# Performance work log

Hardware: AMD Instinct MI355X
Metric: run time of the kernel (lower is better)

Reference implementation:

```python
import jax, jax.numpy as jnp
import numpy as np

B = 8                                   # point clouds per batch
NS = [65536, 16384, 4096, 1024, 256]    # points per scale (stride-4 downsampling)
CS = [32, 64, 128, 256, 512]            # encoder channels per scale
K = 3
BN_EPS = 1e-5


def setup_inputs() -> dict:
    key = jax.random.key(0)
    ks = iter(jax.random.split(key, 64))
    inp = {}
    for i, (n, c) in enumerate(zip(NS, CS)):
        inp[f"p{i}"] = jax.random.uniform(next(ks), (n, 3), jnp.float32)
        inp[f"f{i}"] = jax.random.normal(next(ks), (n, c), jnp.float32)
        inp[f"b{i}"] = jnp.repeat(jnp.arange(B, dtype=jnp.int32), n // B)
    # FP stage mlps: a:(4->3) [768,256,256], b:(3->2) [384,128,128],
    #               c:(2->1) [192,64,64],   d:(1->0) [96,32,32]
    cfg = {"a": (CS[3] + CS[4], CS[3]), "b": (CS[2] + CS[3], CS[2]),
           "c": (CS[1] + CS[2], CS[1]), "d": (CS[0] + CS[1], CS[0])}
    for s, (cin, ch) in cfg.items():
        for j, ci in ((1, cin), (2, ch)):
            inp[f"w{s}{j}"] = jax.random.normal(next(ks), (ci, ch), jnp.float32) / float(np.sqrt(ci))
            inp[f"bias{s}{j}"] = jnp.zeros((ch,), jnp.float32)
            inp[f"g{s}{j}"] = jnp.ones((ch,), jnp.float32)
            inp[f"bt{s}{j}"] = jnp.zeros((ch,), jnp.float32)
    return inp


def _knn_interpolate(x2, p2, p1):
    """torch_geometric.nn.knn_interpolate with k=3; equal-sized sorted batches."""
    n1, n2, c = p1.shape[0] // B, p2.shape[0] // B, x2.shape[1]
    p1b, p2b = p1.reshape(B, n1, 3), p2.reshape(B, n2, 3)
    x2b = x2.reshape(B, n2, c)
    # squared dists via |a|^2 + |b|^2 - 2ab (avoids [B,n1,n2,3] temporary)
    d2 = (jnp.sum(p1b * p1b, -1)[:, :, None] + jnp.sum(p2b * p2b, -1)[:, None, :]
          - 2.0 * jnp.einsum('bnd,bmd->bnm', p1b, p2b))
    neg_d2, idx = jax.lax.top_k(-d2, K)              # [B, n1, K]
    w = 1.0 / jnp.maximum(-neg_d2, 1e-16)            # inverse squared distance
    gath = jax.vmap(lambda x, i: x[i])(x2b, idx)     # [B, n1, K, c]
    out = jnp.einsum('bnk,bnkc->bnc', w, gath) / jnp.sum(w, -1, keepdims=True)
    return out.reshape(B * n1, c)


def _lin_bn_relu(x, w, bias, gamma, beta):
    h = x @ w + bias
    mu = jnp.mean(h, 0)
    var = jnp.mean((h - mu) ** 2, 0)
    return jax.nn.relu((h - mu) * jax.lax.rsqrt(var + BN_EPS) * gamma + beta)


def _fp_stage(p_fine, f_fine, p_coarse, f_coarse, w1, b1, g1, bt1, w2, b2, g2, bt2):
    up = _knn_interpolate(f_coarse, p_coarse, p_fine)
    x = jnp.concatenate([f_fine, up], axis=1)
    x = _lin_bn_relu(x, w1, b1, g1, bt1)
    return _lin_bn_relu(x, w2, b2, g2, bt2)


def reference(p0, p1, p2, p3, p4, f0, f1, f2, f3, f4, b0, b1, b2, b3, b4,
              wa1, biasa1, ga1, bta1, wa2, biasa2, ga2, bta2,
              wb1, biasb1, gb1, btb1, wb2, biasb2, gb2, btb2,
              wc1, biasc1, gc1, btc1, wc2, biasc2, gc2, btc2,
              wd1, biasd1, gd1, btd1, wd2, biasd2, gd2, btd2):
    f3 = _fp_stage(p3, f3, p4, f4, wa1, biasa1, ga1, bta1, wa2, biasa2, ga2, bta2)
    f2 = _fp_stage(p2, f2, p3, f3, wb1, biasb1, gb1, btb1, wb2, biasb2, gb2, btb2)
    f1 = _fp_stage(p1, f1, p2, f2, wc1, biasc1, gc1, btc1, wc2, biasc2, gc2, btc2)
    f0 = _fp_stage(p0, f0, p1, f1, wd1, biasd1, gd1, btd1, wd2, biasd2, gd2, btd2)
    return f0
```

## Files before the change

kernel.cpp:

```cpp
#include <hip/hip_runtime.h>

#define BN_EPS 1e-5f

typedef unsigned short us;

__device__ __forceinline__ float bf2f(us u) {
    union { unsigned int i; float f; } v; v.i = ((unsigned int)u) << 16; return v.f;
}
__device__ __forceinline__ us f2bf(float f) {
    unsigned int x = __float_as_uint(f);
    x += 0x7fffu + ((x >> 16) & 1u);
    return (us)(x >> 16);
}
__device__ __forceinline__ float ldf(const void* p, size_t i, int f32) {
    return f32 ? ((const float*)p)[i] : bf2f(((const us*)p)[i]);
}

__global__ void detect_kernel(const unsigned int* __restrict__ g, int* __restrict__ flag) {
    if (threadIdx.x == 0 && blockIdx.x == 0)
        *flag = ((g[0] & 0xFFFFu) == 0u) ? 1 : 0;
}

__device__ __forceinline__ void lexmerge33(
    const float a0, const int A0, const float a1, const int A1, const float a2, const int A2,
    const float b0, const int B0, const float b1, const int B1, const float b2, const int B2,
    float& m0, int& M0, float& m1, int& M1, float& m2, int& M2)
{
    const bool c1 = (a0 < b0) || (a0 == b0 && A0 < B0);
    m0 = c1 ? a0 : b0;  M0 = c1 ? A0 : B0;
    const float hAd = c1 ? a1 : a0;  const int hAi = c1 ? A1 : A0;
    const float hBd = c1 ? b0 : b1;  const int hBi = c1 ? B0 : B1;
    const bool c2 = (hAd < hBd) || (hAd == hBd && hAi < hBi);
    m1 = c2 ? hAd : hBd;  M1 = c2 ? hAi : hBi;
    const float gAd = c2 ? (c1 ? a2 : a1) : hAd;  const int gAi = c2 ? (c1 ? A2 : A1) : hAi;
    const float gBd = c2 ? hBd : (c1 ? b1 : b2);  const int gBi = c2 ? hBi : (c1 ? B1 : B2);
    const bool c3 = (gAd < gBd) || (gAd == gBd && gAi < gBi);
    m2 = c3 ? gAd : gBd;  M2 = c3 ? gAi : gBi;
}

template<int MODE, int FPB, int SPLIT, int N2>
__global__ __launch_bounds__(FPB * SPLIT)
void knn_up_kernel(
    const void* __restrict__ p_fine,
    const void* __restrict__ p_coarse,
    const void* __restrict__ f_coarse,
    const float* __restrict__ stats,
    const void* __restrict__ gamma,
    const void* __restrict__ beta,
    float inv_n2,
    float* __restrict__ up_out,
    const int* __restrict__ pf32,
    int n2pb, int c2)
{
    constexpr int LEN = N2 / SPLIT;
    constexpr int PSTR = LEN + 4;
    __shared__ __align__(16) float cpx[SPLIT * PSTR];
    __shared__ __align__(16) float cpy[SPLIT * PSTR];
    __shared__ __align__(16) float cpz[SPLIT * PSTR];
    __shared__ __align__(16) float cs2[SPLIT * PSTR];
    __shared__ float aff_a[256], aff_b[256];
    __shared__ int   s_idx[FPB][3];
    __shared__ float s_w[FPB][3];

    const int f32 = *pf32;
    const int tid = threadIdx.x;
    const int cbase = blockIdx.y * n2pb;

    for (int j = tid; j < N2; j += FPB * SPLIT) {
        const size_t b = (size_t)(cbase + j) * 3;
        const float x = ldf(p_coarse, b + 0, f32);
        const float y = ldf(p_coarse, b + 1, f32);
        const float z = ldf(p_coarse, b + 2, f32);
        const int pos = (j / LEN) * PSTR + (j & (LEN - 1));
        cpx[pos] = x; cpy[pos] = y; cpz[pos] = z;
        cs2[pos] = __fadd_rn(__fadd_rn(__fmul_rn(x, x), __fmul_rn(y, y)), __fmul_rn(z, z));
    }
    if (MODE == 1) {
        for (int c = tid; c < c2; c += FPB * SPLIT) {
            float mu  = stats[c] * inv_n2;
            float var = stats[c2 + c] * inv_n2 - mu * mu;
            float a = ldf(gamma, c, f32) * rsqrtf(var + BN_EPS);
            aff_a[c] = a;
            aff_b[c] = ldf(beta, c, f32) - mu * a;
        }
    }
    __syncthreads();

    {
        const int f = tid / SPLIT;
        const int s = tid & (SPLIT - 1);
        const int row = (blockIdx.y * gridDim.x + blockIdx.x) * FPB + f;
        const size_t b = (size_t)row * 3;
        const float px = ldf(p_fine, b + 0, f32);
        const float py = ldf(p_fine, b + 1, f32);
        const float pz = ldf(p_fine, b + 2, f32);
        const float s1 = __fadd_rn(__fadd_rn(__fmul_rn(px, px), __fmul_rn(py, py)),
                                   __fmul_rn(pz, pz));
        const int jb = s * LEN;
        const int base = s * PSTR;
        float t0 = 1e30f, t1 = 1e30f, t2 = 1e30f;
        int i0 = jb, i1 = jb, i2 = jb;
        for (int t = 0; t < LEN; t += 4) {
            const float4 X = *(const float4*)&cpx[base + t];
            const float4 Y = *(const float4*)&cpy[base + t];
            const float4 Z = *(const float4*)&cpz[base + t];
            const float4 S = *(const float4*)&cs2[base + t];
            #pragma unroll
            for (int q = 0; q < 4; ++q) {
                const float qx = ((const float*)&X)[q];
                const float qy = ((const float*)&Y)[q];
                const float qz = ((const float*)&Z)[q];
                const float s2 = ((const float*)&S)[q];
                const float dot = fmaf(pz, qz, fmaf(py, qy, __fmul_rn(px, qx)));
                const float d = __fsub_rn(__fadd_rn(s1, s2), __fmul_rn(2.0f, dot));
                const int jj = jb + t + q;
                const bool a0 = d < t0, a1 = d < t1, a2 = d < t2;
                t2 = a1 ? t1 : (a2 ? d : t2);  i2 = a1 ? i1 : (a2 ? jj : i2);
                t1 = a0 ? t0 : (a1 ? d : t1);  i1 = a0 ? i0 : (a1 ? jj : i1);
                t0 = a0 ? d  : t0;             i0 = a0 ? jj : i0;
            }
        }

        #pragma unroll
        for (int m = 1; m < SPLIT; m <<= 1) {
            const float o0 = __shfl_xor(t0, m, 64); const int oi0 = __shfl_xor(i0, m, 64);
            const float o1 = __shfl_xor(t1, m, 64); const int oi1 = __shfl_xor(i1, m, 64);
            const float o2 = __shfl_xor(t2, m, 64); const int oi2 = __shfl_xor(i2, m, 64);
            float n0, n1, n2v; int ni0, ni1, ni2;
            lexmerge33(t0, i0, t1, i1, t2, i2,
                       o0, oi0, o1, oi1, o2, oi2,
                       n0, ni0, n1, ni1, n2v, ni2);
            t0 = n0; i0 = ni0; t1 = n1; i1 = ni1; t2 = n2v; i2 = ni2;
        }
        if (s == 0) {
            s_idx[f][0] = cbase + i0;  s_w[f][0] = __fdiv_rn(1.0f, fmaxf(t0, 1e-16f));
            s_idx[f][1] = cbase + i1;  s_w[f][1] = __fdiv_rn(1.0f, fmaxf(t1, 1e-16f));
            s_idx[f][2] = cbase + i2;  s_w[f][2] = __fdiv_rn(1.0f, fmaxf(t2, 1e-16f));
        }
    }
    __syncthreads();

    const int lane = tid & 63, wv = tid >> 6;
    const int nw = (FPB * SPLIT) / 64;
    for (int p = wv; p < FPB; p += nw) {
        const int row = (blockIdx.y * gridDim.x + blockIdx.x) * FPB + p;
        const int g0 = s_idx[p][0], g1 = s_idx[p][1], g2 = s_idx[p][2];
        const float w0 = s_w[p][0], w1 = s_w[p][1], w2 = s_w[p][2];
        const float den = __fadd_rn(__fadd_rn(w0, w1), w2);
        float* __restrict__ urow = up_out + (size_t)row * c2;
        for (int c = lane; c < c2; c += 64) {
            float v0, v1, v2;
            if (MODE == 0) {
                v0 = ldf(f_coarse, (size_t)g0 * c2 + c, f32);
                v1 = ldf(f_coarse, (size_t)g1 * c2 + c, f32);
                v2 = ldf(f_coarse, (size_t)g2 * c2 + c, f32);
            } else {
                const float* fc = (const float*)f_coarse;
                const float aa = aff_a[c], bb = aff_b[c];
                v0 = fmaxf(aa * fc[(size_t)g0 * c2 + c] + bb, 0.f);
                v1 = fmaxf(aa * fc[(size_t)g1 * c2 + c] + bb, 0.f);
                v2 = fmaxf(aa * fc[(size_t)g2 * c2 + c] + bb, 0.f);
            }
            const float num = fmaf(w2, v2, fmaf(w1, v1, __fmul_rn(w0, v0)));
            urow[c] = __fdiv_rn(num, den);
        }
    }
}

__global__ __launch_bounds__(256)
void gemm1_bn_kernel(const void* __restrict__ Ffine,
                     const float* __restrict__ Up,
                     const void* __restrict__ W,
                     const void* __restrict__ bias,
                     float* __restrict__ H,
                     float* __restrict__ stats_out,
                     const int* __restrict__ pf32,
                     int M, int c1, int c2, int N)
{
    __shared__ __align__(16) float As[16][68];
    __shared__ __align__(16) float Bs[16][68];
    __shared__ float s_sum[64], s_sq[64];

    const int f32 = *pf32;
    const int K = c1 + c2;
    const int tid = threadIdx.x;
    const int tx = tid & 15, ty = tid >> 4;
    const int n0 = blockIdx.x * 64, m0 = blockIdx.y * 64;

    if (tid < 64) { s_sum[tid] = 0.f; s_sq[tid] = 0.f; }

    const int a_m = tid >> 2;
    const int a_k = (tid & 3) << 2;
    const int b_k = tid >> 4;
    const int b_n = (tid & 15) << 2;
    const int row = m0 + a_m;

    float avp[4]; float4 bvp;
    {
        const int k = a_k;
        if (k < c1) {
            if (f32) {
                const float4 v = *(const float4*)((const float*)Ffine + (size_t)row * c1 + k);
                avp[0] = v.x; avp[1] = v.y; avp[2] = v.z; avp[3] = v.w;
            } else {
                const ushort4 u = *(const ushort4*)((const us*)Ffine + (size_t)row * c1 + k);
                avp[0] = bf2f(u.x); avp[1] = bf2f(u.y); avp[2] = bf2f(u.z); avp[3] = bf2f(u.w);
            }
        } else {
            const float4 v = *(const float4*)(Up + (size_t)row * c2 + (k - c1));
            avp[0] = v.x; avp[1] = v.y; avp[2] = v.z; avp[3] = v.w;
        }
        bvp = make_float4(0.f, 0.f, 0.f, 0.f);
        if (n0 + b_n < N) {
            const size_t wi = (size_t)b_k * N + (n0 + b_n);
            if (f32) bvp = *(const float4*)((const float*)W + wi);
            else {
                const ushort4 u = *(const ushort4*)((const us*)W + wi);
                bvp = make_float4(bf2f(u.x), bf2f(u.y), bf2f(u.z), bf2f(u.w));
            }
        }
    }

    float acc[4][4] = {};

    for (int k0 = 0; k0 < K; k0 += 16) {
        #pragma unroll
        for (int i = 0; i < 4; ++i) As[a_k + i][a_m] = avp[i];
        *(float4*)&Bs[b_k][b_n] = bvp;
        __syncthreads();

        float avn[4]; float4 bvn;
        const int kn = k0 + 16;
        if (kn < K) {
            const int k = kn + a_k;
            if (k < c1) {
                if (f32) {
                    const float4 v = *(const float4*)((const float*)Ffine + (size_t)row * c1 + k);
                    avn[0] = v.x; avn[1] = v.y; avn[2] = v.z; avn[3] = v.w;
                } else {
                    const ushort4 u = *(const ushort4*)((const us*)Ffine + (size_t)row * c1 + k);
                    avn[0] = bf2f(u.x); avn[1] = bf2f(u.y); avn[2] = bf2f(u.z); avn[3] = bf2f(u.w);
                }
            } else {
                const float4 v = *(const float4*)(Up + (size_t)row * c2 + (k - c1));
                avn[0] = v.x; avn[1] = v.y; avn[2] = v.z; avn[3] = v.w;
            }
            bvn = make_float4(0.f, 0.f, 0.f, 0.f);
            if (n0 + b_n < N) {
                const size_t wi = (size_t)(kn + b_k) * N + (n0 + b_n);
                if (f32) bvn = *(const float4*)((const float*)W + wi);
                else {
                    const ushort4 u = *(const ushort4*)((const us*)W + wi);
                    bvn = make_float4(bf2f(u.x), bf2f(u.y), bf2f(u.z), bf2f(u.w));
                }
            }
        }

        #pragma unroll
        for (int kk = 0; kk < 16; ++kk) {
            const float4 a4 = *(const float4*)&As[kk][ty << 2];
            const float4 b4 = *(const float4*)&Bs[kk][tx << 2];
            const float aarr[4] = {a4.x, a4.y, a4.z, a4.w};
            const float barr[4] = {b4.x, b4.y, b4.z, b4.w};
            #pragma unroll
            for (int i = 0; i < 4; ++i)
                #pragma unroll
                for (int j = 0; j < 4; ++j)
                    acc[i][j] = fmaf(aarr[i], barr[j], acc[i][j]);
        }
        __syncthreads();

        if (kn < K) {
            #pragma unroll
            for (int i = 0; i < 4; ++i) avp[i] = avn[i];
            bvp = bvn;
        }
    }

    float bvals[4];
    const bool colsok = (n0 + (tx << 2)) < N;
    #pragma unroll
    for (int j = 0; j < 4; ++j) {
        const int n = n0 + (tx << 2) + j;
        bvals[j] = (n < N) ? ldf(bias, n, f32) : 0.f;
    }
    float ps[4] = {0.f, 0.f, 0.f, 0.f}, pq[4] = {0.f, 0.f, 0.f, 0.f};
    #pragma unroll
    for (int i = 0; i < 4; ++i) {
        float4 hv;
        float* hvp = (float*)&hv;
        #pragma unroll
        for (int j = 0; j < 4; ++j) {
            const float v = acc[i][j] + bvals[j];
            hvp[j] = v;
            ps[j] += v;
            pq[j] = fmaf(v, v, pq[j]);
        }
        if (colsok)
            *(float4*)(H + (size_t)(m0 + (ty << 2) + i) * N + n0 + (tx << 2)) = hv;
    }
    #pragma unroll
    for (int j = 0; j < 4; ++j) {
        atomicAdd(&s_sum[(tx << 2) + j], ps[j]);
        atomicAdd(&s_sq[(tx << 2) + j], pq[j]);
    }
    __syncthreads();
    if (tid < 64) {
        const int n = n0 + tid;
        if (n < N) {
            atomicAdd(&stats_out[n], s_sum[tid]);
            atomicAdd(&stats_out[N + n], s_sq[tid]);
        }
    }
}

__global__ __launch_bounds__(256)
void gemm2_bn_kernel(const float* __restrict__ A,
                     const void* __restrict__ W,
                     const void* __restrict__ bias,
                     const float* __restrict__ stats_in,
                     const void* __restrict__ g_in,
                     const void* __restrict__ bt_in,
                     float inv_m,
                     float* __restrict__ H,
                     float* __restrict__ stats_out,
                     const int* __restrict__ pf32,
                     int M, int K, int N)
{
    __shared__ __align__(16) float As[16][68];
    __shared__ __align__(16) float Bs[16][68];
    __shared__ float aff_a[256], aff_b[256];
    __shared__ float s_sum[64], s_sq[64];

    const int f32 = *pf32;
    const int tid = threadIdx.x;
    const int tx = tid & 15, ty = tid >> 4;
    const int n0 = blockIdx.x * 64, m0 = blockIdx.y * 64;

    for (int c = tid; c < K; c += 256) {
        float mu  = stats_in[c] * inv_m;
        float var = stats_in[K + c] * inv_m - mu * mu;
        float a = ldf(g_in, c, f32) * rsqrtf(var + BN_EPS);
        aff_a[c] = a; aff_b[c] = ldf(bt_in, c, f32) - mu * a;
    }
    if (tid < 64) { s_sum[tid] = 0.f; s_sq[tid] = 0.f; }
    __syncthreads();

    const int a_m = tid >> 2;
    const int a_k = (tid & 3) << 2;
    const int b_k = tid >> 4;
    const int b_n = (tid & 15) << 2;
    const int row = m0 + a_m;

    float avp[4]; float4 bvp;
    {
        const float4 af = *(const float4*)(A + (size_t)row * K + a_k);
        avp[0] = af.x; avp[1] = af.y; avp[2] = af.z; avp[3] = af.w;
        bvp = make_float4(0.f, 0.f, 0.f, 0.f);
        if (n0 + b_n < N) {
            const size_t wi = (size_t)b_k * N + (n0 + b_n);
            if (f32) bvp = *(const float4*)((const float*)W + wi);
            else {
                const ushort4 u = *(const ushort4*)((const us*)W + wi);
                bvp = make_float4(bf2f(u.x), bf2f(u.y), bf2f(u.z), bf2f(u.w));
            }
        }
    }

    float acc[4][4] = {};

    for (int k0 = 0; k0 < K; k0 += 16) {
        #pragma unroll
        for (int i = 0; i < 4; ++i)
            As[a_k + i][a_m] = fmaxf(fmaf(aff_a[k0 + a_k + i], avp[i], aff_b[k0 + a_k + i]), 0.f);
        *(float4*)&Bs[b_k][b_n] = bvp;
        __syncthreads();

        float avn[4]; float4 bvn;
        const int kn = k0 + 16;
        if (kn < K) {
            const float4 af = *(const float4*)(A + (size_t)row * K + (kn + a_k));
            avn[0] = af.x; avn[1] = af.y; avn[2] = af.z; avn[3] = af.w;
            bvn = make_float4(0.f, 0.f, 0.f, 0.f);
            if (n0 + b_n < N) {
                const size_t wi = (size_t)(kn + b_k) * N + (n0 + b_n);
                if (f32) bvn = *(const float4*)((const float*)W + wi);
                else {
                    const ushort4 u = *(const ushort4*)((const us*)W + wi);
                    bvn = make_float4(bf2f(u.x), bf2f(u.y), bf2f(u.z), bf2f(u.w));
                }
            }
        }

        #pragma unroll
        for (int kk = 0; kk < 16; ++kk) {
            const float4 a4 = *(const float4*)&As[kk][ty << 2];
            const float4 b4 = *(const float4*)&Bs[kk][tx << 2];
            const float aarr[4] = {a4.x, a4.y, a4.z, a4.w};
            const float barr[4] = {b4.x, b4.y, b4.z, b4.w};
            #pragma unroll
            for (int i = 0; i < 4; ++i)
                #pragma unroll
                for (int j = 0; j < 4; ++j)
                    acc[i][j] = fmaf(aarr[i], barr[j], acc[i][j]);
        }
        __syncthreads();

        if (kn < K) {
            #pragma unroll
            for (int i = 0; i < 4; ++i) avp[i] = avn[i];
            bvp = bvn;
        }
    }

    float bvals[4];
    const bool colsok = (n0 + (tx << 2)) < N;
    #pragma unroll
    for (int j = 0; j < 4; ++j) {
        const int n = n0 + (tx << 2) + j;
        bvals[j] = (n < N) ? ldf(bias, n, f32) : 0.f;
    }
    float ps[4] = {0.f, 0.f, 0.f, 0.f}, pq[4] = {0.f, 0.f, 0.f, 0.f};
    #pragma unroll
    for (int i = 0; i < 4; ++i) {
        float4 hv;
        float* hvp = (float*)&hv;
        #pragma unroll
        for (int j = 0; j < 4; ++j) {
            const float v = acc[i][j] + bvals[j];
            hvp[j] = v;
            ps[j] += v;
            pq[j] = fmaf(v, v, pq[j]);
        }
        if (colsok)
            *(float4*)(H + (size_t)(m0 + (ty << 2) + i) * N + n0 + (tx << 2)) = hv;
    }
    #pragma unroll
    for (int j = 0; j < 4; ++j) {
        atomicAdd(&s_sum[(tx << 2) + j], ps[j]);
        atomicAdd(&s_sq[(tx << 2) + j], pq[j]);
    }
    __syncthreads();
    if (tid < 64) {
        const int n = n0 + tid;
        if (n < N) {
            atomicAdd(&stats_out[n], s_sum[tid]);
            atomicAdd(&stats_out[N + n], s_sq[tid]);
        }
    }
}

__global__ __launch_bounds__(256)
void finalize_kernel(const float* __restrict__ Hf, const float* __restrict__ stats,
                     const void* __restrict__ g, const void* __restrict__ bt,
                     float inv_m, void* __restrict__ out,
                     const int* __restrict__ pf32, int total)
{
    const int idx = blockIdx.x * 256 + threadIdx.x;
    if (idx >= total) return;
    const int f32 = *pf32;
    const int c = idx & 31;
    const float mu  = stats[c] * inv_m;
    const float var = stats[32 + c] * inv_m - mu * mu;
    const float a = ldf(g, c, f32) * rsqrtf(var + BN_EPS);
    const float b = ldf(bt, c, f32) - mu * a;
    const float v = fmaxf(fmaf(a, Hf[idx], b), 0.f);
    if (f32) ((float*)out)[idx] = v;
    else     ((us*)out)[idx] = f2bf(v);
}

extern "C" void kernel_launch(void* const* d_in, const int* in_sizes, int n_in,
                              void* d_out, int out_size, void* d_ws, size_t ws_size,
                              hipStream_t stream) {
    (void)in_sizes; (void)n_in; (void)out_size; (void)ws_size;
    const void* p0 = d_in[0];
    const void* f0 = d_in[1];
    const void* p1 = d_in[3];
    const void* f1 = d_in[4];
    const void* p2 = d_in[6];
    const void* f2 = d_in[7];
    const void* p3 = d_in[9];
    const void* f3 = d_in[10];
    const void* p4 = d_in[12];
    const void* f4 = d_in[13];
    const void *W1[4], *B1[4], *G1[4], *T1[4], *W2[4], *B2[4], *G2[4], *T2[4];
    for (int s = 0; s < 4; ++s) {
        const int b = 15 + s * 8;
        W1[s] = d_in[b + 0]; B1[s] = d_in[b + 1];
        G1[s] = d_in[b + 2]; T1[s] = d_in[b + 3];
        W2[s] = d_in[b + 4]; B2[s] = d_in[b + 5];
        G2[s] = d_in[b + 6]; T2[s] = d_in[b + 7];
    }

    float* stats = (float*)d_ws;
    float* st_a1 = stats + 0;
    float* st_a2 = stats + 512;
    float* st_b1 = stats + 1024;
    float* st_b2 = stats + 1280;
    float* st_c1 = stats + 1536;
    float* st_c2 = stats + 1664;
    float* st_d1 = stats + 1792;
    float* st_d2 = stats + 1856;
    int*   flag  = (int*)(stats + 1920);
    float* U = (float*)((char*)d_ws + 8192);
    float* H = U + 4194304;
    float* h2a = H + 262144;
    float* h2b = H + 524288;
    float* h2c = H + 1048576;
    float* h2d = U;

    hipMemsetAsync(d_ws, 0, 1920 * sizeof(float), stream);
    detect_kernel<<<1, 64, 0, stream>>>((const unsigned int*)G1[0], flag);

    knn_up_kernel<0, 64, 4, 32><<<dim3(2, 8), 256, 0, stream>>>(
        p3, p4, f4, nullptr, nullptr, nullptr, 0.f, U, flag, 32, 512);
    gemm1_bn_kernel<<<dim3(4, 16), 256, 0, stream>>>(
        f3, U, W1[0], B1[0], H, st_a1, flag, 1024, 256, 512, 256);
    gemm2_bn_kernel<<<dim3(4, 16), 256, 0, stream>>>(
        H, W2[0], B2[0], st_a1, G1[0], T1[0], 1.f / 1024.f,
        h2a, st_a2, flag, 1024, 256, 256);
    knn_up_kernel<1, 64, 4, 128><<<dim3(8, 8), 256, 0, stream>>>(
        p2, p3, h2a, st_a2, G2[0], T2[0], 1.f / 1024.f, U, flag, 128, 256);
    gemm1_bn_kernel<<<dim3(2, 64), 256, 0, stream>>>(
        f2, U, W1[1], B1[1], H, st_b1, flag, 4096, 128, 256, 128);
    gemm2_bn_kernel<<<dim3(2, 64), 256, 0, stream>>>(
        H, W2[1], B2[1], st_b1, G1[1], T1[1], 1.f / 4096.f,
        h2b, st_b2, flag, 4096, 128, 128);
    knn_up_kernel<1, 32, 16, 512><<<dim3(64, 8), 512, 0, stream>>>(
        p1, p2, h2b, st_b2, G2[1], T2[1], 1.f / 4096.f, U, flag, 512, 128);
    gemm1_bn_kernel<<<dim3(1, 256), 256, 0, stream>>>(
        f1, U, W1[2], B1[2], H, st_c1, flag, 16384, 64, 128, 64);
    gemm2_bn_kernel<<<dim3(1, 256), 256, 0, stream>>>(
        H, W2[2], B2[2], st_c1, G1[2], T1[2], 1.f / 16384.f,
        h2c, st_c2, flag, 16384, 64, 64);
    knn_up_kernel<1, 64, 8, 2048><<<dim3(128, 8), 512, 0, stream>>>(
        p0, p1, h2c, st_c2, G2[2], T2[2], 1.f / 16384.f, U, flag, 2048, 64);
    gemm1_bn_kernel<<<dim3(1, 1024), 256, 0, stream>>>(
        f0, U, W1[3], B1[3], H, st_d1, flag, 65536, 32, 64, 32);
    gemm2_bn_kernel<<<dim3(1, 1024), 256, 0, stream>>>(
        H, W2[3], B2[3], st_d1, G1[3], T1[3], 1.f / 65536.f,
        h2d, st_d2, flag, 65536, 32, 32);
    finalize_kernel<<<(65536 * 32) / 256, 256, 0, stream>>>(
        h2d, st_d2, G2[3], T2[3], 1.f / 65536.f, d_out, flag, 65536 * 32);
}
```

Measured before the change: 514.2 us.

## Precompute coarse points as AoS float4 and restructure KNN per-wave scan

Adds a prep kernel that packs the coarse points into a float4 array (2x, 2y, 2z, |p|^2), so the KNN inner loop reads one broadcast global load per candidate instead of staging four LDS arrays per block. Each wave now owns 64 fine points with one lane per point and scans its own slice of candidates with register prefetch. Slices are then merged through shared memory by the first wave rather than by cross-lane shuffles. This trades redundant per-block coordinate staging for extra launches, a serial final merge in one wave, and uniform global loads that rely on the cache.

```diff
diff --git a/kernel.cpp b/kernel.cpp
--- a/kernel.cpp
+++ b/kernel.cpp
@@ -19,6 +19,20 @@
 __global__ void detect_kernel(const unsigned int* __restrict__ g, int* __restrict__ flag) {
     if (threadIdx.x == 0 && blockIdx.x == 0)
         *flag = ((g[0] & 0xFFFFu) == 0u) ? 1 : 0;
+}
+
+__global__ __launch_bounds__(256)
+void prep_aos_kernel(const void* __restrict__ p, float4* __restrict__ aos,
+                     const int* __restrict__ pf32, int n)
+{
+    const int i = blockIdx.x * 256 + threadIdx.x;
+    if (i >= n) return;
+    const int f32 = *pf32;
+    const float x = ldf(p, (size_t)3 * i + 0, f32);
+    const float y = ldf(p, (size_t)3 * i + 1, f32);
+    const float z = ldf(p, (size_t)3 * i + 2, f32);
+    const float s2 = __fadd_rn(__fadd_rn(__fmul_rn(x, x), __fmul_rn(y, y)), __fmul_rn(z, z));
+    aos[i] = make_float4(__fadd_rn(x, x), __fadd_rn(y, y), __fadd_rn(z, z), s2);
 }
 
 __device__ __forceinline__ void lexmerge33(
@@ -38,11 +52,11 @@
     m2 = c3 ? gAd : gBd;  M2 = c3 ? gAi : gBi;
 }
 
-template<int MODE, int FPB, int SPLIT, int N2>
-__global__ __launch_bounds__(FPB * SPLIT)
+template<int MODE, int SPLIT, int LEN>
+__global__ __launch_bounds__(64 * SPLIT, 8)
 void knn_up_kernel(
     const void* __restrict__ p_fine,
-    const void* __restrict__ p_coarse,
+    const float4* __restrict__ aos,
     const void* __restrict__ f_coarse,
     const float* __restrict__ stats,
     const void* __restrict__ gamma,
@@ -52,31 +66,21 @@
     const int* __restrict__ pf32,
     int n2pb, int c2)
 {
-    constexpr int LEN = N2 / SPLIT;
-    constexpr int PSTR = LEN + 4;
-    __shared__ __align__(16) float cpx[SPLIT * PSTR];
-    __shared__ __align__(16) float cpy[SPLIT * PSTR];
-    __shared__ __align__(16) float cpz[SPLIT * PSTR];
-    __shared__ __align__(16) float cs2[SPLIT * PSTR];
+    __shared__ float mrg_d[SPLIT * 64 * 3];
+    __shared__ int   mrg_i[SPLIT * 64 * 3];
     __shared__ float aff_a[256], aff_b[256];
-    __shared__ int   s_idx[FPB][3];
-    __shared__ float s_w[FPB][3];
+    __shared__ int   s_idx[64][3];
+    __shared__ float s_w[64][3];
 
     const int f32 = *pf32;
     const int tid = threadIdx.x;
+    const int lane = tid & 63;
+    const int wv = tid >> 6;
     const int cbase = blockIdx.y * n2pb;
-
-    for (int j = tid; j < N2; j += FPB * SPLIT) {
-        const size_t b = (size_t)(cbase + j) * 3;
-        const float x = ldf(p_coarse, b + 0, f32);
-        const float y = ldf(p_coarse, b + 1, f32);
-        const float z = ldf(p_coarse, b + 2, f32);
-        const int pos = (j / LEN) * PSTR + (j & (LEN - 1));
-        cpx[pos] = x; cpy[pos] = y; cpz[pos] = z;
-        cs2[pos] = __fadd_rn(__fadd_rn(__fmul_rn(x, x), __fmul_rn(y, y)), __fmul_rn(z, z));
-    }
+    const int row0 = (blockIdx.y * gridDim.x + blockIdx.x) * 64;
+
     if (MODE == 1) {
-        for (int c = tid; c < c2; c += FPB * SPLIT) {
+        for (int c = tid; c < c2; c += 64 * SPLIT) {
             float mu  = stats[c] * inv_n2;
             float var = stats[c2 + c] * inv_n2 - mu * mu;
             float a = ldf(gamma, c, f32) * rsqrtf(var + BN_EPS);
@@ -84,66 +88,72 @@
             aff_b[c] = ldf(beta, c, f32) - mu * a;
         }
     }
-    __syncthreads();
 
     {
-        const int f = tid / SPLIT;
-        const int s = tid & (SPLIT - 1);
-        const int row = (blockIdx.y * gridDim.x + blockIdx.x) * FPB + f;
+        const int row = row0 + lane;
         const size_t b = (size_t)row * 3;
         const float px = ldf(p_fine, b + 0, f32);
         const float py = ldf(p_fine, b + 1, f32);
         const float pz = ldf(p_fine, b + 2, f32);
         const float s1 = __fadd_rn(__fadd_rn(__fmul_rn(px, px), __fmul_rn(py, py)),
                                    __fmul_rn(pz, pz));
-        const int jb = s * LEN;
-        const int base = s * PSTR;
+        const int jb = wv * LEN;
+        const float4* __restrict__ sl = aos + cbase + jb;
         float t0 = 1e30f, t1 = 1e30f, t2 = 1e30f;
         int i0 = jb, i1 = jb, i2 = jb;
+
+#define KNN_UPD(CQ, JJ) {                                                     \
+        const float dot2 = fmaf(pz, (CQ).z, fmaf(py, (CQ).y,                  \
+                                __fmul_rn(px, (CQ).x)));                      \
+        const float d = __fsub_rn(__fadd_rn(s1, (CQ).w), dot2);               \
+        const int jj = (JJ);                                                  \
+        const bool a0 = d < t0, a1 = d < t1, a2 = d < t2;                     \
+        t2 = a1 ? t1 : (a2 ? d : t2);  i2 = a1 ? i1 : (a2 ? jj : i2);         \
+        t1 = a0 ? t0 : (a1 ? d : t1);  i1 = a0 ? i0 : (a1 ? jj : i1);         \
+        t0 = a0 ? d  : t0;             i0 = a0 ? jj : i0; }
+
+        float4 ca = sl[0], cb = sl[1], cc = sl[2], cd = sl[3];
         for (int t = 0; t < LEN; t += 4) {
-            const float4 X = *(const float4*)&cpx[base + t];
-            const float4 Y = *(const float4*)&cpy[base + t];
-            const float4 Z = *(const float4*)&cpz[base + t];
-            const float4 S = *(const float4*)&cs2[base + t];
-            #pragma unroll
-            for (int q = 0; q < 4; ++q) {
-                const float qx = ((const float*)&X)[q];
-                const float qy = ((const float*)&Y)[q];
-                const float qz = ((const float*)&Z)[q];
-                const float s2 = ((const float*)&S)[q];
-                const float dot = fmaf(pz, qz, fmaf(py, qy, __fmul_rn(px, qx)));
-                const float d = __fsub_rn(__fadd_rn(s1, s2), __fmul_rn(2.0f, dot));
-                const int jj = jb + t + q;
-                const bool a0 = d < t0, a1 = d < t1, a2 = d < t2;
-                t2 = a1 ? t1 : (a2 ? d : t2);  i2 = a1 ? i1 : (a2 ? jj : i2);
-                t1 = a0 ? t0 : (a1 ? d : t1);  i1 = a0 ? i0 : (a1 ? jj : i1);
-                t0 = a0 ? d  : t0;             i0 = a0 ? jj : i0;
-            }
-        }
-
-        #pragma unroll
-        for (int m = 1; m < SPLIT; m <<= 1) {
-            const float o0 = __shfl_xor(t0, m, 64); const int oi0 = __shfl_xor(i0, m, 64);
-            const float o1 = __shfl_xor(t1, m, 64); const int oi1 = __shfl_xor(i1, m, 64);
-            const float o2 = __shfl_xor(t2, m, 64); const int oi2 = __shfl_xor(i2, m, 64);
+            float4 na, nb, nc, nd;
+            const bool more = (t + 4) < LEN;
+            if (more) { na = sl[t + 4]; nb = sl[t + 5]; nc = sl[t + 6]; nd = sl[t + 7]; }
+            KNN_UPD(ca, jb + t + 0);
+            KNN_UPD(cb, jb + t + 1);
+            KNN_UPD(cc, jb + t + 2);
+            KNN_UPD(cd, jb + t + 3);
+            if (more) { ca = na; cb = nb; cc = nc; cd = nd; }
+        }
+#undef KNN_UPD
+
+        const int mb = (wv * 64 + lane) * 3;
+        mrg_d[mb + 0] = t0;  mrg_i[mb + 0] = cbase + i0;
+        mrg_d[mb + 1] = t1;  mrg_i[mb + 1] = cbase + i1;
+        mrg_d[mb + 2] = t2;  mrg_i[mb + 2] = cbase + i2;
+    }
+    __syncthreads();
+
+    if (tid < 64) {
+        float d0 = mrg_d[tid * 3 + 0], d1 = mrg_d[tid * 3 + 1], d2 = mrg_d[tid * 3 + 2];
+        int   j0 = mrg_i[tid * 3 + 0], j1 = mrg_i[tid * 3 + 1], j2 = mrg_i[tid * 3 + 2];
+        #pragma unroll
+        for (int w = 1; w < SPLIT; ++w) {
+            const int mb = (w * 64 + tid) * 3;
+            const float e0 = mrg_d[mb + 0], e1 = mrg_d[mb + 1], e2 = mrg_d[mb + 2];
+            const int   k0 = mrg_i[mb + 0], k1 = mrg_i[mb + 1], k2 = mrg_i[mb + 2];
             float n0, n1, n2v; int ni0, ni1, ni2;
-            lexmerge33(t0, i0, t1, i1, t2, i2,
-                       o0, oi0, o1, oi1, o2, oi2,
+            lexmerge33(d0, j0, d1, j1, d2, j2,
+                       e0, k0, e1, k1, e2, k2,
                        n0, ni0, n1, ni1, n2v, ni2);
-            t0 = n0; i0 = ni0; t1 = n1; i1 = ni1; t2 = n2v; i2 = ni2;
-        }
-        if (s == 0) {
-            s_idx[f][0] = cbase + i0;  s_w[f][0] = __fdiv_rn(1.0f, fmaxf(t0, 1e-16f));
-            s_idx[f][1] = cbase + i1;  s_w[f][1] = __fdiv_rn(1.0f, fmaxf(t1, 1e-16f));
-            s_idx[f][2] = cbase + i2;  s_w[f][2] = __fdiv_rn(1.0f, fmaxf(t2, 1e-16f));
-        }
+            d0 = n0; j0 = ni0; d1 = n1; j1 = ni1; d2 = n2v; j2 = ni2;
+        }
+        s_idx[tid][0] = j0;  s_w[tid][0] = __fdiv_rn(1.0f, fmaxf(d0, 1e-16f));
+        s_idx[tid][1] = j1;  s_w[tid][1] = __fdiv_rn(1.0f, fmaxf(d1, 1e-16f));
+        s_idx[tid][2] = j2;  s_w[tid][2] = __fdiv_rn(1.0f, fmaxf(d2, 1e-16f));
     }
     __syncthreads();
 
-    const int lane = tid & 63, wv = tid >> 6;
-    const int nw = (FPB * SPLIT) / 64;
-    for (int p = wv; p < FPB; p += nw) {
-        const int row = (blockIdx.y * gridDim.x + blockIdx.x) * FPB + p;
+    for (int p = wv; p < 64; p += SPLIT) {
+        const int row = row0 + p;
         const int g0 = s_idx[p][0], g1 = s_idx[p][1], g2 = s_idx[p][2];
         const float w0 = s_w[p][0], w1 = s_w[p][1], w2 = s_w[p][2];
         const float den = __fadd_rn(__fadd_rn(w0, w1), w2);
@@ -508,33 +518,38 @@
     float* h2b = H + 524288;
     float* h2c = H + 1048576;
     float* h2d = U;
+    float4* aosbuf = (float4*)H;
 
     hipMemsetAsync(d_ws, 0, 1920 * sizeof(float), stream);
     detect_kernel<<<1, 64, 0, stream>>>((const unsigned int*)G1[0], flag);
 
-    knn_up_kernel<0, 64, 4, 32><<<dim3(2, 8), 256, 0, stream>>>(
-        p3, p4, f4, nullptr, nullptr, nullptr, 0.f, U, flag, 32, 512);
+    prep_aos_kernel<<<1, 256, 0, stream>>>(p4, aosbuf, flag, 256);
+    knn_up_kernel<0, 8, 4><<<dim3(2, 8), 512, 0, stream>>>(
+        p3, aosbuf, f4, nullptr, nullptr, nullptr, 0.f, U, flag, 32, 512);
     gemm1_bn_kernel<<<dim3(4, 16), 256, 0, stream>>>(
         f3, U, W1[0], B1[0], H, st_a1, flag, 1024, 256, 512, 256);
     gemm2_bn_kernel<<<dim3(4, 16), 256, 0, stream>>>(
         H, W2[0], B2[0], st_a1, G1[0], T1[0], 1.f / 1024.f,
         h2a, st_a2, flag, 1024, 256, 256);
-    knn_up_kernel<1, 64, 4, 128><<<dim3(8, 8), 256, 0, stream>>>(
-        p2, p3, h2a, st_a2, G2[0], T2[0], 1.f / 1024.f, U, flag, 128, 256);
+    prep_aos_kernel<<<4, 256, 0, stream>>>(p3, aosbuf, flag, 1024);
+    knn_up_kernel<1, 8, 16><<<dim3(8, 8), 512, 0, stream>>>(
+        p2, aosbuf, h2a, st_a2, G2[0], T2[0], 1.f / 1024.f, U, flag, 128, 256);
     gemm1_bn_kernel<<<dim3(2, 64), 256, 0, stream>>>(
         f2, U, W1[1], B1[1], H, st_b1, flag, 4096, 128, 256, 128);
     gemm2_bn_kernel<<<dim3(2, 64), 256, 0, stream>>>(
         H, W2[1], B2[1], st_b1, G1[1], T1[1], 1.f / 4096.f,
         h2b, st_b2, flag, 4096, 128, 128);
-    knn_up_kernel<1, 32, 16, 512><<<dim3(64, 8), 512, 0, stream>>>(
-        p1, p2, h2b, st_b2, G2[1], T2[1], 1.f / 4096.f, U, flag, 512, 128);
+    prep_aos_kernel<<<16, 256, 0, stream>>>(p2, aosbuf, flag, 4096);
+    knn_up_kernel<1, 16, 32><<<dim3(32, 8), 1024, 0, stream>>>(
+        p1, aosbuf, h2b, st_b2, G2[1], T2[1], 1.f / 4096.f, U, flag, 512, 128);
     gemm1_bn_kernel<<<dim3(1, 256), 256, 0, stream>>>(
         f1, U, W1[2], B1[2], H, st_c1, flag, 16384, 64, 128, 64);
     gemm2_bn_kernel<<<dim3(1, 256), 256, 0, stream>>>(
         H, W2[2], B2[2], st_c1, G1[2], T1[2], 1.f / 16384.f,
         h2c, st_c2, flag, 16384, 64, 64);
-    knn_up_kernel<1, 64, 8, 2048><<<dim3(128, 8), 512, 0, stream>>>(
-        p0, p1, h2c, st_c2, G2[2], T2[2], 1.f / 16384.f, U, flag, 2048, 64);
+    prep_aos_kernel<<<64, 256, 0, stream>>>(p1, aosbuf, flag, 16384);
+    knn_up_kernel<1, 8, 256><<<dim3(128, 8), 512, 0, stream>>>(
+        p0, aosbuf, h2c, st_c2, G2[2], T2[2], 1.f / 16384.f, U, flag, 2048, 64);
     gemm1_bn_kernel<<<dim3(1, 1024), 256, 0, stream>>>(
         f0, U, W1[3], B1[3], H, st_d1, flag, 65536, 32, 64, 32);
     gemm2_bn_kernel<<<dim3(1, 1024), 256, 0, stream>>>(
```

Result: faster. 500.5 us, median of 3 (-2.7%).
